# Kernel tuning notes

Hardware: AMD Instinct MI355X
Metric: run time of the kernel (lower is better)

## Reference

```python
import jax, jax.numpy as jnp
import numpy as np

SIGMA = 1.0
RADIUS = 4        # int(truncate * sigma + 0.5), skimage default truncate=4.0
NBINS = 256       # skimage threshold_otsu default
MEAN, STD = 0.5, 0.5


def _gauss_kernel():
    xs = np.arange(-RADIUS, RADIUS + 1, dtype=np.float32)
    k = np.exp(-0.5 * (xs / SIGMA) ** 2)
    return jnp.asarray(k / k.sum())


def _blur(img):
    # img: [B, H, W]; skimage gaussian(sigma=1) == separable conv, 'nearest' (edge) padding
    k = _gauss_kernel()
    p = jnp.pad(img, ((0, 0), (RADIUS, RADIUS), (RADIUS, RADIUS)), mode='edge')
    x = p[:, None]  # [B,1,H+2R,W+2R]
    x = jax.lax.conv_general_dilated(x, k.reshape(1, 1, -1, 1), (1, 1), 'VALID')
    x = jax.lax.conv_general_dilated(x, k.reshape(1, 1, 1, -1), (1, 1), 'VALID')
    return x[:, 0]


def _otsu(img):
    # Otsu threshold over a 256-bin histogram spanning [min, max] (skimage semantics)
    mn, mx = img.min(), img.max()
    rng = jnp.maximum(mx - mn, 1e-12)
    idx = jnp.clip(jnp.floor((img - mn) / rng * NBINS).astype(jnp.int32), 0, NBINS - 1)
    hist = jnp.zeros(NBINS, jnp.float32).at[idx.ravel()].add(1.0)
    centers = mn + (jnp.arange(NBINS, dtype=jnp.float32) + 0.5) * (rng / NBINS)
    w1 = jnp.cumsum(hist)
    w2 = jnp.cumsum(hist[::-1])[::-1]
    m1 = jnp.cumsum(hist * centers) / jnp.maximum(w1, 1e-12)
    m2 = jnp.cumsum((hist * centers)[::-1])[::-1] / jnp.maximum(w2, 1e-12)
    var12 = w1[:-1] * w2[1:] * (m1[:-1] - m2[1:]) ** 2
    return centers[jnp.argmax(var12)]


def setup_inputs() -> dict:
    key = jax.random.key(0)
    x = jax.random.normal(key, (32, 4, 512, 512), dtype=jnp.float32)
    return {"x": x}


def reference(x):
    # thershold_mask on thermal channel: denormalize (mul std, add mean), clamp, blur, Otsu
    thermal = jnp.clip(x[:, 0] * STD + MEAN, 0.0, 1.0)          # [B,H,W]
    blurred = _blur(thermal)                                     # [B,H,W]
    t = jax.vmap(_otsu)(blurred)                                 # [B]
    mask = jnp.where(blurred > t[:, None, None], 1.0, blurred)   # soft mask
    # rgba2rgb with white background: out = alpha*rgb + (1-alpha)*1, clipped to [0,1]
    rgb = x[:, -3:]                                              # [B,3,H,W]
    alpha = mask[:, None]                                        # [B,1,H,W]
    out_rgb = jnp.clip(alpha * rgb + (1.0 - alpha), 0.0, 1.0)
    # use_thermal=True: replace last 3 channels, keep thermal channel
    return x.at[:, 1:4].set(out_rgb)
```

## Files before the change

kernel.cpp:

```cpp
#include <hip/hip_runtime.h>
#include <math.h>

#define NIMG 32
#define HWDIM 512
#define NPIX (HWDIM * HWDIM)
#define NB 256
#define RAD 4
#define TW 64
#define TH 64

struct W9 { float w[9]; };

__device__ __forceinline__ float clip01(float v) { return fminf(fmaxf(v, 0.0f), 1.0f); }

static float np_expf(float x) {
  const float LOG2E = 1.442695040f;
  const float CW_HI = -6.93145752e-1f;
  const float CW_LO = -1.42860677e-6f;
  const float P0 = 9.999999999980870924916e-01f;
  const float P1 = 7.257664613233124478488e-01f;
  const float P2 = 2.473615434895520810817e-01f;
  const float P3 = 5.114512081637298353406e-02f;
  const float P4 = 6.757896990527504603057e-03f;
  const float P5 = 5.082762527590693718096e-04f;
  const float Q0 = 1.000000000000000000000e+00f;
  const float Q1 = -2.742335390411667452936e-01f;
  const float Q2 = 2.159509375685829852307e-02f;
  float m = rintf(x * LOG2E);
  float y = fmaf(m, CW_HI, x);
  y = fmaf(m, CW_LO, y);
  float num = fmaf(fmaf(fmaf(fmaf(fmaf(P5, y, P4), y, P3), y, P2), y, P1), y, P0);
  float den = fmaf(fmaf(Q2, y, Q1), y, Q0);
  float r = num / den;
  return ldexpf(r, (int)m);
}

__global__ __launch_bounds__(256) void init_kernel(int* __restrict__ minI, int* __restrict__ maxI,
                                                   int* __restrict__ hist) {
  int tid = blockIdx.x * blockDim.x + threadIdx.x;
  if (tid < NIMG) { minI[tid] = 0x7F800000; maxI[tid] = 0; }
  int stride = gridDim.x * blockDim.x;
  for (int i = tid; i < NIMG * NB; i += stride) hist[i] = 0;
}

__global__ __launch_bounds__(256) void blur_kernel(const float* __restrict__ x, float* __restrict__ out,
                                                   int* __restrict__ minI, int* __restrict__ maxI, W9 wp) {
  __shared__ float raw[TH + 8][TW + 8];
  __shared__ float vb[TH][TW + 8];
  const int img = blockIdx.z;
  const int tx0 = blockIdx.x * TW;
  const int ty0 = blockIdx.y * TH;
  const float* src = x + (size_t)img * 4 * NPIX;
  float* out0 = out + (size_t)img * 4 * NPIX;
  float* bl = out0 + NPIX;
  const int tid = threadIdx.x;

  for (int i = tid; i < (TH + 8) * (TW + 8); i += 256) {
    int lr = i / (TW + 8), lc = i % (TW + 8);
    int gr = ty0 - RAD + lr; gr = gr < 0 ? 0 : (gr > HWDIM - 1 ? HWDIM - 1 : gr);
    int gc = tx0 - RAD + lc; gc = gc < 0 ? 0 : (gc > HWDIM - 1 ? HWDIM - 1 : gc);
    float v = src[gr * HWDIM + gc];
    if (lr >= RAD && lr < RAD + TH && lc >= RAD && lc < RAD + TW)
      out0[gr * HWDIM + gc] = v;
    raw[lr][lc] = clip01(__fadd_rn(__fmul_rn(v, 0.5f), 0.5f));
  }
  __syncthreads();

  for (int i = tid; i < TH * (TW + 8); i += 256) {
    int r = i / (TW + 8), c = i % (TW + 8);
    double acc = 0.0;
#pragma unroll
    for (int k = 0; k < 9; ++k) acc += (double)wp.w[k] * (double)raw[r + k][c];
    vb[r][c] = (float)acc;
  }
  __syncthreads();

  float lmn = __int_as_float(0x7F800000);
  float lmx = 0.0f;
  for (int i = tid; i < TH * TW; i += 256) {
    int r = i >> 6, c = i & 63;
    double acc = 0.0;
#pragma unroll
    for (int k = 0; k < 9; ++k) acc += (double)wp.w[k] * (double)vb[r][c + k];
    float a = (float)acc;
    bl[(ty0 + r) * HWDIM + (tx0 + c)] = a;
    lmn = fminf(lmn, a);
    lmx = fmaxf(lmx, a);
  }
  for (int off = 32; off > 0; off >>= 1) {
    lmn = fminf(lmn, __shfl_down(lmn, off, 64));
    lmx = fmaxf(lmx, __shfl_down(lmx, off, 64));
  }
  __shared__ float smn[4], smx[4];
  if ((tid & 63) == 0) { smn[tid >> 6] = lmn; smx[tid >> 6] = lmx; }
  __syncthreads();
  if (tid == 0) {
    float mnb = fminf(fminf(smn[0], smn[1]), fminf(smn[2], smn[3]));
    float mxb = fmaxf(fmaxf(smx[0], smx[1]), fmaxf(smx[2], smx[3]));
    atomicMin(&minI[img], __float_as_int(mnb));
    atomicMax(&maxI[img], __float_as_int(mxb));
  }
}

__global__ __launch_bounds__(256) void hist_kernel(const float* __restrict__ out, const int* __restrict__ minI,
                                                   const int* __restrict__ maxI, int* __restrict__ hist) {
  __shared__ int lh[4 * 260];
  const int img = blockIdx.y;
  const int tid = threadIdx.x;
  for (int i = tid; i < 4 * 260; i += 256) lh[i] = 0;
  __syncthreads();
  const float mn = __int_as_float(minI[img]);
  const float mx = __int_as_float(maxI[img]);
  const float rng = fmaxf(mx - mn, 1e-12f);
  const float4* src = (const float4*)(out + (size_t)img * 4 * NPIX + NPIX);
  int* my = lh + (tid & 3) * 260;
#pragma unroll
  for (int j = 0; j < 4; ++j) {
    float4 v = src[blockIdx.x * 1024 + j * 256 + tid];
    float q; int b;
    q = __fmul_rn(__fdiv_rn(__fsub_rn(v.x, mn), rng), 256.0f); b = (int)floorf(q); b = b < 0 ? 0 : (b > 255 ? 255 : b); atomicAdd(&my[b], 1);
    q = __fmul_rn(__fdiv_rn(__fsub_rn(v.y, mn), rng), 256.0f); b = (int)floorf(q); b = b < 0 ? 0 : (b > 255 ? 255 : b); atomicAdd(&my[b], 1);
    q = __fmul_rn(__fdiv_rn(__fsub_rn(v.z, mn), rng), 256.0f); b = (int)floorf(q); b = b < 0 ? 0 : (b > 255 ? 255 : b); atomicAdd(&my[b], 1);
    q = __fmul_rn(__fdiv_rn(__fsub_rn(v.w, mn), rng), 256.0f); b = (int)floorf(q); b = b < 0 ? 0 : (b > 255 ? 255 : b); atomicAdd(&my[b], 1);
  }
  __syncthreads();
  int c = lh[tid] + lh[260 + tid] + lh[2 * 260 + tid] + lh[3 * 260 + tid];
  if (c) atomicAdd(&hist[img * NB + tid], c);
}

__global__ __launch_bounds__(64) void otsu_kernel(const int* __restrict__ hist, const int* __restrict__ minI,
                                                  const int* __restrict__ maxI, float* __restrict__ t) {
  __shared__ int h[NB];
  __shared__ float rs[NB + 1];
  const int img = blockIdx.x;
  const int tid = threadIdx.x;
  for (int i = tid; i < NB; i += 64) h[i] = hist[img * NB + i];
  __syncthreads();
  if (tid != 0) return;

  const float mn = __int_as_float(minI[img]);
  const float mx = __int_as_float(maxI[img]);
  const float rng = fmaxf(mx - mn, 1e-12f);
  const float scale = rng / 256.0f;

  float acc = 0.0f;
  rs[NB] = 0.0f;
  for (int i = NB - 1; i >= 0; --i) {
    float c = __fadd_rn(mn, __fmul_rn((float)i + 0.5f, scale));
    acc = __fadd_rn(acc, __fmul_rn((float)h[i], c));
    rs[i] = acc;
  }

  float w1 = 0.0f, cs1 = 0.0f, best = -INFINITY;
  int arg = 0;
  for (int i = 0; i < NB - 1; ++i) {
    float hi = (float)h[i];
    float c = __fadd_rn(mn, __fmul_rn((float)i + 0.5f, scale));
    w1 = __fadd_rn(w1, hi);
    cs1 = __fadd_rn(cs1, __fmul_rn(hi, c));
    float w2n = (float)NPIX - w1;
    float m1 = __fdiv_rn(cs1, fmaxf(w1, 1e-12f));
    float m2n = __fdiv_rn(rs[i + 1], fmaxf(w2n, 1e-12f));
    float d = __fsub_rn(m1, m2n);
    float v = __fmul_rn(__fmul_rn(w1, w2n), __fmul_rn(d, d));
    if (v > best) { best = v; arg = i; }
  }
  t[img] = __fadd_rn(mn, __fmul_rn((float)arg + 0.5f, scale));
}

__global__ __launch_bounds__(256) void mask_kernel(const float* __restrict__ x, const float* __restrict__ tarr,
                                                   float* __restrict__ out) {
  const int gid = blockIdx.x * 256 + threadIdx.x;
  const int img = gid >> 16;
  const int rem = gid & 65535;
  const float4* xb = (const float4*)(x + (size_t)img * 4 * NPIX);
  float4* ob = (float4*)(out + (size_t)img * 4 * NPIX);
  const float tv = tarr[img];

  float4 bl = ob[65536 + rem];
  float4 x1 = xb[65536 + rem];
  float4 x2 = xb[2 * 65536 + rem];
  float4 x3 = xb[3 * 65536 + rem];

  float a0 = bl.x > tv ? 1.0f : bl.x;
  float a1 = bl.y > tv ? 1.0f : bl.y;
  float a2 = bl.z > tv ? 1.0f : bl.z;
  float a3 = bl.w > tv ? 1.0f : bl.w;

  float4 o1, o2, o3;
  o1.x = clip01(__fadd_rn(__fmul_rn(a0, x1.x), 1.0f - a0));
  o1.y = clip01(__fadd_rn(__fmul_rn(a1, x1.y), 1.0f - a1));
  o1.z = clip01(__fadd_rn(__fmul_rn(a2, x1.z), 1.0f - a2));
  o1.w = clip01(__fadd_rn(__fmul_rn(a3, x1.w), 1.0f - a3));
  o2.x = clip01(__fadd_rn(__fmul_rn(a0, x2.x), 1.0f - a0));
  o2.y = clip01(__fadd_rn(__fmul_rn(a1, x2.y), 1.0f - a1));
  o2.z = clip01(__fadd_rn(__fmul_rn(a2, x2.z), 1.0f - a2));
  o2.w = clip01(__fadd_rn(__fmul_rn(a3, x2.w), 1.0f - a3));
  o3.x = clip01(__fadd_rn(__fmul_rn(a0, x3.x), 1.0f - a0));
  o3.y = clip01(__fadd_rn(__fmul_rn(a1, x3.y), 1.0f - a1));
  o3.z = clip01(__fadd_rn(__fmul_rn(a2, x3.z), 1.0f - a2));
  o3.w = clip01(__fadd_rn(__fmul_rn(a3, x3.w), 1.0f - a3));

  ob[65536 + rem] = o1;
  ob[2 * 65536 + rem] = o2;
  ob[3 * 65536 + rem] = o3;
}

extern "C" void kernel_launch(void* const* d_in, const int* in_sizes, int n_in,
                              void* d_out, int out_size, void* d_ws, size_t ws_size,
                              hipStream_t stream) {
  const float* x = (const float*)d_in[0];
  float* out = (float*)d_out;
  char* ws = (char*)d_ws;
  int* minI = (int*)(ws + 0);
  int* maxI = (int*)(ws + 128);
  int* hist = (int*)(ws + 256);
  float* t = (float*)(ws + 256 + NIMG * NB * 4);

  W9 wp;
  {
    float k[9];
    for (int i = 0; i < 9; ++i) {
      float xs = (float)(i - 4);
      float argv = -0.5f * (xs * xs);
      k[i] = np_expf(argv);
    }
    float s = ((k[0] + k[1]) + (k[2] + k[3])) + ((k[4] + k[5]) + (k[6] + k[7]));
    s = s + k[8];
    for (int i = 0; i < 9; ++i) wp.w[i] = k[i] / s;
  }

  hipLaunchKernelGGL(init_kernel, dim3(33), dim3(256), 0, stream, minI, maxI, hist);
  hipLaunchKernelGGL(blur_kernel, dim3(HWDIM / TW, HWDIM / TH, NIMG), dim3(256), 0, stream,
                     x, out, minI, maxI, wp);
  hipLaunchKernelGGL(hist_kernel, dim3(NPIX / 16 / 256, NIMG), dim3(256), 0, stream,
                     out, minI, maxI, hist);
  hipLaunchKernelGGL(otsu_kernel, dim3(NIMG), dim3(64), 0, stream, hist, minI, maxI, t);
  hipLaunchKernelGGL(mask_kernel, dim3(NIMG * NPIX / 4 / 256), dim3(256), 0, stream,
                     x, t, out);
}
```

Before: 146.4 us.

## Replace global atomics and init kernel with per-block partial min/max and histograms

Drops the init kernel and the global atomics for min/max and histogram accumulation. Each blur block writes its own min/max to the workspace, and each histogram block writes a partial histogram into scratch space in the output buffer. Downstream kernels reduce these partials themselves. This removes one launch and atomic contention, at the cost of redundant reductions in the hist and otsu kernels and reliance on output channel 2 as scratch until mask_kernel overwrites it.

```diff
diff --git a/kernel.cpp b/kernel.cpp
--- a/kernel.cpp
+++ b/kernel.cpp
@@ -35,19 +35,12 @@
   return ldexpf(r, (int)m);
 }
 
-__global__ __launch_bounds__(256) void init_kernel(int* __restrict__ minI, int* __restrict__ maxI,
-                                                   int* __restrict__ hist) {
-  int tid = blockIdx.x * blockDim.x + threadIdx.x;
-  if (tid < NIMG) { minI[tid] = 0x7F800000; maxI[tid] = 0; }
-  int stride = gridDim.x * blockDim.x;
-  for (int i = tid; i < NIMG * NB; i += stride) hist[i] = 0;
-}
-
 __global__ __launch_bounds__(256) void blur_kernel(const float* __restrict__ x, float* __restrict__ out,
-                                                   int* __restrict__ minI, int* __restrict__ maxI, W9 wp) {
+                                                   float* __restrict__ mnmx, W9 wp) {
   __shared__ float raw[TH + 8][TW + 8];
   __shared__ float vb[TH][TW + 8];
   const int img = blockIdx.z;
+  const int blk = blockIdx.y * 8 + blockIdx.x;
   const int tx0 = blockIdx.x * TW;
   const int ty0 = blockIdx.y * TH;
   const float* src = x + (size_t)img * 4 * NPIX;
@@ -97,26 +90,42 @@
   if (tid == 0) {
     float mnb = fminf(fminf(smn[0], smn[1]), fminf(smn[2], smn[3]));
     float mxb = fmaxf(fmaxf(smx[0], smx[1]), fmaxf(smx[2], smx[3]));
-    atomicMin(&minI[img], __float_as_int(mnb));
-    atomicMax(&maxI[img], __float_as_int(mxb));
-  }
-}
-
-__global__ __launch_bounds__(256) void hist_kernel(const float* __restrict__ out, const int* __restrict__ minI,
-                                                   const int* __restrict__ maxI, int* __restrict__ hist) {
+    mnmx[img * 128 + blk * 2] = mnb;
+    mnmx[img * 128 + blk * 2 + 1] = mxb;
+  }
+}
+
+__global__ __launch_bounds__(256) void hist_kernel(const float* __restrict__ mnmx, float* __restrict__ out) {
   __shared__ int lh[4 * 260];
+  __shared__ float s_mn, s_mx;
   const int img = blockIdx.y;
+  const int p = blockIdx.x;
   const int tid = threadIdx.x;
   for (int i = tid; i < 4 * 260; i += 256) lh[i] = 0;
-  __syncthreads();
-  const float mn = __int_as_float(minI[img]);
-  const float mx = __int_as_float(maxI[img]);
+
+  float lmn = __int_as_float(0x7F800000);
+  float lmx = 0.0f;
+  if (tid < 64) {
+    lmn = mnmx[img * 128 + tid * 2];
+    lmx = mnmx[img * 128 + tid * 2 + 1];
+  }
+  if (tid < 64) {
+    for (int off = 32; off > 0; off >>= 1) {
+      lmn = fminf(lmn, __shfl_down(lmn, off, 64));
+      lmx = fmaxf(lmx, __shfl_down(lmx, off, 64));
+    }
+    if (tid == 0) { s_mn = lmn; s_mx = lmx; }
+  }
+  __syncthreads();
+  const float mn = s_mn;
+  const float mx = s_mx;
   const float rng = fmaxf(mx - mn, 1e-12f);
+
   const float4* src = (const float4*)(out + (size_t)img * 4 * NPIX + NPIX);
   int* my = lh + (tid & 3) * 260;
 #pragma unroll
   for (int j = 0; j < 4; ++j) {
-    float4 v = src[blockIdx.x * 1024 + j * 256 + tid];
+    float4 v = src[p * 1024 + j * 256 + tid];
     float q; int b;
     q = __fmul_rn(__fdiv_rn(__fsub_rn(v.x, mn), rng), 256.0f); b = (int)floorf(q); b = b < 0 ? 0 : (b > 255 ? 255 : b); atomicAdd(&my[b], 1);
     q = __fmul_rn(__fdiv_rn(__fsub_rn(v.y, mn), rng), 256.0f); b = (int)floorf(q); b = b < 0 ? 0 : (b > 255 ? 255 : b); atomicAdd(&my[b], 1);
@@ -125,21 +134,39 @@
   }
   __syncthreads();
   int c = lh[tid] + lh[260 + tid] + lh[2 * 260 + tid] + lh[3 * 260 + tid];
-  if (c) atomicAdd(&hist[img * NB + tid], c);
-}
-
-__global__ __launch_bounds__(64) void otsu_kernel(const int* __restrict__ hist, const int* __restrict__ minI,
-                                                  const int* __restrict__ maxI, float* __restrict__ t) {
+  int* part = (int*)(out + (size_t)img * 4 * NPIX + 2 * NPIX);
+  part[p * NB + tid] = c;
+}
+
+__global__ __launch_bounds__(256) void otsu_kernel(const float* __restrict__ mnmx, const float* __restrict__ out,
+                                                   float* __restrict__ t) {
   __shared__ int h[NB];
   __shared__ float rs[NB + 1];
+  __shared__ float s_mn, s_mx;
   const int img = blockIdx.x;
   const int tid = threadIdx.x;
-  for (int i = tid; i < NB; i += 64) h[i] = hist[img * NB + i];
+  const int* part = (const int*)(out + (size_t)img * 4 * NPIX + 2 * NPIX);
+  int sum = 0;
+#pragma unroll 8
+  for (int p = 0; p < 64; ++p) sum += part[p * NB + tid];
+  h[tid] = sum;
+
+  float lmn = __int_as_float(0x7F800000);
+  float lmx = 0.0f;
+  if (tid < 64) {
+    lmn = mnmx[img * 128 + tid * 2];
+    lmx = mnmx[img * 128 + tid * 2 + 1];
+    for (int off = 32; off > 0; off >>= 1) {
+      lmn = fminf(lmn, __shfl_down(lmn, off, 64));
+      lmx = fmaxf(lmx, __shfl_down(lmx, off, 64));
+    }
+    if (tid == 0) { s_mn = lmn; s_mx = lmx; }
+  }
   __syncthreads();
   if (tid != 0) return;
 
-  const float mn = __int_as_float(minI[img]);
-  const float mx = __int_as_float(maxI[img]);
+  const float mn = s_mn;
+  const float mx = s_mx;
   const float rng = fmaxf(mx - mn, 1e-12f);
   const float scale = rng / 256.0f;
 
@@ -212,10 +239,8 @@
   const float* x = (const float*)d_in[0];
   float* out = (float*)d_out;
   char* ws = (char*)d_ws;
-  int* minI = (int*)(ws + 0);
-  int* maxI = (int*)(ws + 128);
-  int* hist = (int*)(ws + 256);
-  float* t = (float*)(ws + 256 + NIMG * NB * 4);
+  float* mnmx = (float*)(ws + 0);
+  float* t = (float*)(ws + 32 * 128 * 4);
 
   W9 wp;
   {
@@ -230,12 +255,10 @@
     for (int i = 0; i < 9; ++i) wp.w[i] = k[i] / s;
   }
 
-  hipLaunchKernelGGL(init_kernel, dim3(33), dim3(256), 0, stream, minI, maxI, hist);
   hipLaunchKernelGGL(blur_kernel, dim3(HWDIM / TW, HWDIM / TH, NIMG), dim3(256), 0, stream,
-                     x, out, minI, maxI, wp);
-  hipLaunchKernelGGL(hist_kernel, dim3(NPIX / 16 / 256, NIMG), dim3(256), 0, stream,
-                     out, minI, maxI, hist);
-  hipLaunchKernelGGL(otsu_kernel, dim3(NIMG), dim3(64), 0, stream, hist, minI, maxI, t);
+                     x, out, mnmx, wp);
+  hipLaunchKernelGGL(hist_kernel, dim3(64, NIMG), dim3(256), 0, stream, mnmx, out);
+  hipLaunchKernelGGL(otsu_kernel, dim3(NIMG), dim3(256), 0, stream, mnmx, out, t);
   hipLaunchKernelGGL(mask_kernel, dim3(NIMG * NPIX / 4 / 256), dim3(256), 0, stream,
                      x, t, out);
 }
```

Result: faster. 134.6 us (-8.1%).
